# Kernel optimization log

Hardware: AMD Instinct MI355X
Metric: run time of the kernel (lower is better)

Reference implementation:

```python
import jax, jax.numpy as jnp
import numpy as np

N_NODES = 50000
N_EDGES = 600000
N_PAIRS = 200000
D_IN, D_HID = 128, 256


def _sage_conv(x, src, dst, W_l, b_l, W_r, num_nodes):
    # PyG SAGEConv('mean'): out = mean_agg(x_j) @ W_l + b_l + x @ W_r
    msgs = x[src]                                              # [E, d] gather
    agg = jax.ops.segment_sum(msgs, dst, num_segments=num_nodes)
    deg = jax.ops.segment_sum(jnp.ones((src.shape[0],), x.dtype), dst,
                              num_segments=num_nodes)
    agg = agg / jnp.maximum(deg, 1.0)[:, None]                 # mean, safe for deg=0
    return agg @ W_l + b_l + x @ W_r


def setup_inputs() -> dict:
    key = jax.random.key(0)
    ks = jax.random.split(key, 8)
    s = lambda d: 1.0 / np.sqrt(d)
    return {
        "features": jax.random.normal(ks[0], (N_NODES, D_IN), jnp.float32),
        "edge_index": jax.random.randint(ks[1], (2, N_EDGES), 0, N_NODES, jnp.int64),
        "mask": jax.random.randint(ks[2], (N_PAIRS, 2), 0, N_NODES, jnp.int64),
        "W1l": jax.random.normal(ks[3], (D_IN, D_HID), jnp.float32) * s(D_IN),
        "b1l": jnp.zeros((D_HID,), jnp.float32),
        "W1r": jax.random.normal(ks[4], (D_IN, D_HID), jnp.float32) * s(D_IN),
        "W2l": jax.random.normal(ks[5], (D_HID, D_IN), jnp.float32) * s(D_HID),
        "b2l": jnp.zeros((D_IN,), jnp.float32),
        "W2r": jax.random.normal(ks[6], (D_HID, D_IN), jnp.float32) * s(D_HID),
        "Wlin": jax.random.normal(ks[7], (2 * D_IN, 1), jnp.float32) * s(2 * D_IN),
        "blin": jnp.zeros((1,), jnp.float32),
    }


def reference(features, edge_index, mask, W1l, b1l, W1r, W2l, b2l, W2r, Wlin, blin):
    n = features.shape[0]
    src, dst = edge_index[0], edge_index[1]
    h = _sage_conv(features, src, dst, W1l, b1l, W1r, n)       # [N, 256]
    h = jax.nn.relu(h)                                         # dropout p=0 -> identity
    h = _sage_conv(h, src, dst, W2l, b2l, W2r, n)              # [N, 128]
    m = mask.T                                                 # [2, P]
    p1 = jax.lax.stop_gradient(h[m[0]])                        # detach in original
    p2 = jax.lax.stop_gradient(h[m[1]])
    pair = jnp.concatenate((p1, p2), axis=1)                   # [P, 256]
    return jax.nn.sigmoid(pair @ Wlin + blin)                  # [P, 1]
```

## Files before the change

kernel.cpp:

```cpp
#include <hip/hip_runtime.h>
#include <math.h>

#define NN 50000
#define NE 600000
#define NP 200000
#define NB_SCAN 49

typedef unsigned int uint;
typedef unsigned short ushort;
typedef __attribute__((ext_vector_type(8))) short bf16x8;
typedef __attribute__((ext_vector_type(4))) float f32x4;

__device__ __forceinline__ ushort f2bf(float f) {
    uint u = __float_as_uint(f);
    uint r = (u + 0x7FFFu + ((u >> 16) & 1u)) >> 16;
    return (ushort)r;
}
__device__ __forceinline__ float bf2f(uint lo16) {
    return __uint_as_float(lo16 << 16);
}

__device__ __forceinline__ int wave_iscan(int v, int lane) {
#pragma unroll
    for (int off = 1; off < 64; off <<= 1) {
        int t = __shfl_up(v, off, 64);
        if (lane >= off) v += t;
    }
    return v;
}

template <int K, int N>
__device__ __forceinline__ void prepB_one(int idx, const float* __restrict__ Wt,
                                          const float* __restrict__ Wb,
                                          ushort* __restrict__ Bp) {
    int lane = idx & 63;
    int nt = (idx >> 6) % (N / 16);
    int ct = idx / (64 * (N / 16));
    int n = nt * 16 + (lane & 15);
    int kb = ct * 32 + (lane >> 4) * 8;
#pragma unroll
    for (int j = 0; j < 8; j++) {
        int k = kb + j;
        float w = (k < K / 2) ? Wt[(size_t)k * N + n] : Wb[(size_t)(k - K / 2) * N + n];
        Bp[(size_t)idx * 8 + j] = f2bf(w);
    }
}

#define T_PREP (NN * 64)
#define T_DEG  (T_PREP + NE)
#define T_B1   (T_DEG + 8192)
#define T_PQ   (T_B1 + 1024)
#define T_CAB  (T_PQ + 2)
__global__ void k_pre(const float* __restrict__ x, uint* __restrict__ A1u,
                      const int* __restrict__ dst, int* __restrict__ deg,
                      const float* __restrict__ W1l, const float* __restrict__ W1r,
                      ushort* __restrict__ Bp1,
                      const float* __restrict__ W2l, const float* __restrict__ W2r,
                      const float* __restrict__ Wlin, const float* __restrict__ b2l,
                      float* __restrict__ pq, float* __restrict__ cab) {
    int t = blockIdx.x * 256 + threadIdx.x;
    if (t < T_PREP) {
        int n = t >> 6, c2 = t & 63;
        float2 v = *(const float2*)(x + (size_t)n * 128 + c2 * 2);
        A1u[(size_t)n * 128 + 64 + c2] = (uint)f2bf(v.x) | ((uint)f2bf(v.y) << 16);
    } else if (t < T_DEG) {
        atomicAdd(deg + dst[t - T_PREP], 1);
    } else if (t < T_B1) {
        prepB_one<256, 256>(t - T_DEG, W1l, W1r, Bp1);
    } else if (t < T_PQ) {
        int idx = t - T_B1;
        int vec = idx >> 8;
        int k = idx & 255;
        const float* W = (vec < 2) ? W2l : W2r;
        const float* wl = Wlin + (vec & 1) * 128;
        float s = 0.f;
#pragma unroll 4
        for (int j = 0; j < 128; j++) s += W[(size_t)k * 128 + j] * wl[j];
        pq[idx] = s;
    } else if (t < T_CAB) {
        int i = t - T_PQ;
        float s = 0.f;
        for (int j = 0; j < 128; j++) s += b2l[j] * Wlin[i * 128 + j];
        cab[i] = s;
    }
}

__global__ __launch_bounds__(1024) void k_scan1(const int* __restrict__ deg,
                                                int* __restrict__ excl,
                                                int* __restrict__ bsum) {
    int tid = threadIdx.x;
    int i = blockIdx.x * 1024 + tid;
    int lane = tid & 63, wid = tid >> 6;
    int v = (i < NN) ? deg[i] : 0;
    int incl = wave_iscan(v, lane);
    __shared__ int wt[16];
    if (lane == 63) wt[wid] = incl;
    __syncthreads();
    if (tid < 16) {
        int w = wt[tid];
#pragma unroll
        for (int off = 1; off < 16; off <<= 1) {
            int t = __shfl_up(w, off, 64);
            if (tid >= off) w += t;
        }
        wt[tid] = w;
    }
    __syncthreads();
    int base = (wid > 0) ? wt[wid - 1] : 0;
    if (i < NN) excl[i] = incl - v + base;
    if (tid == 0) bsum[blockIdx.x] = wt[15];
}

__global__ void k_scan2(int* __restrict__ bsum) {
    int lane = threadIdx.x;
    int v = (lane < NB_SCAN) ? bsum[lane] : 0;
    int incl = wave_iscan(v, lane);
    if (lane < NB_SCAN) bsum[lane] = incl - v;
}

__global__ __launch_bounds__(1024) void k_scan3(const int* __restrict__ excl,
                                                const int* __restrict__ bsum,
                                                int* __restrict__ rowptr,
                                                int* __restrict__ cursor) {
    int i = blockIdx.x * 1024 + threadIdx.x;
    if (i < NN) {
        int v = excl[i] + bsum[blockIdx.x];
        rowptr[i] = v;
        cursor[i] = v;
    }
    if (i == 0) rowptr[NN] = NE;
}

__global__ void k_fill(const int* __restrict__ src, const int* __restrict__ dst,
                       int* __restrict__ cursor, int* __restrict__ ssrc) {
    int e = blockIdx.x * 256 + threadIdx.x;
    if (e >= NE) return;
    int d = dst[e];
    int pos = atomicAdd(cursor + d, 1);
    ssrc[pos] = src[e];
}

__global__ void k_agg1(uint* __restrict__ A1u, const int* __restrict__ rowptr,
                       const int* __restrict__ ssrc) {
    int t = blockIdx.x * 256 + threadIdx.x;
    int n = t >> 6;
    if (n >= NN) return;
    int lane = t & 63;
    int r0 = rowptr[n], r1 = rowptr[n + 1];
    float ax0 = 0.f, ay0 = 0.f, ax1 = 0.f, ay1 = 0.f;
    float ax2 = 0.f, ay2 = 0.f, ax3 = 0.f, ay3 = 0.f;
    int e = r0;
    for (; e + 4 <= r1; e += 4) {
        int s0 = ssrc[e], s1 = ssrc[e + 1], s2 = ssrc[e + 2], s3 = ssrc[e + 3];
        uint v0 = A1u[(size_t)s0 * 128 + 64 + lane];
        uint v1 = A1u[(size_t)s1 * 128 + 64 + lane];
        uint v2 = A1u[(size_t)s2 * 128 + 64 + lane];
        uint v3 = A1u[(size_t)s3 * 128 + 64 + lane];
        ax0 += bf2f(v0 & 0xffffu); ay0 += bf2f(v0 >> 16);
        ax1 += bf2f(v1 & 0xffffu); ay1 += bf2f(v1 >> 16);
        ax2 += bf2f(v2 & 0xffffu); ay2 += bf2f(v2 >> 16);
        ax3 += bf2f(v3 & 0xffffu); ay3 += bf2f(v3 >> 16);
    }
    for (; e < r1; e++) {
        int s = ssrc[e];
        uint v = A1u[(size_t)s * 128 + 64 + lane];
        ax0 += bf2f(v & 0xffffu); ay0 += bf2f(v >> 16);
    }
    float ax = (ax0 + ax1) + (ax2 + ax3);
    float ay = (ay0 + ay1) + (ay2 + ay3);
    float sc = 1.0f / fmaxf((float)(r1 - r0), 1.0f);
    A1u[(size_t)n * 128 + lane] = (uint)f2bf(ax * sc) | ((uint)f2bf(ay * sc) << 16);
}

__global__ __launch_bounds__(256) void k_gemm1(const ushort* __restrict__ A,
                                               const ushort* __restrict__ Bp,
                                               const float* __restrict__ bias,
                                               const float* __restrict__ pq,
                                               float2* __restrict__ g2,
                                               float2* __restrict__ u2) {
    const int K = 256, NTW = 4;
    int wave = threadIdx.x >> 6;
    int lane = threadIdx.x & 63;
    int quad = lane >> 4;
    int l15 = lane & 15;
    int mbase = blockIdx.x * 32;
    int r0 = mbase + l15;       if (r0 >= NN) r0 = NN - 1;
    int r1 = mbase + 16 + l15;  if (r1 >= NN) r1 = NN - 1;
    f32x4 acc0[NTW], acc1[NTW];
#pragma unroll
    for (int i = 0; i < NTW; i++) {
        acc0[i] = (f32x4){0.f, 0.f, 0.f, 0.f};
        acc1[i] = (f32x4){0.f, 0.f, 0.f, 0.f};
    }
    const bf16x8* bp = (const bf16x8*)Bp;
#pragma unroll
    for (int ct = 0; ct < K / 32; ct++) {
        bf16x8 a0 = *(const bf16x8*)(A + (size_t)r0 * K + ct * 32 + quad * 8);
        bf16x8 a1 = *(const bf16x8*)(A + (size_t)r1 * K + ct * 32 + quad * 8);
#pragma unroll
        for (int ntl = 0; ntl < NTW; ntl++) {
            int nt = wave * NTW + ntl;
            bf16x8 b = bp[(ct * 16 + nt) * 64 + lane];
            acc0[ntl] = __builtin_amdgcn_mfma_f32_16x16x32_bf16(a0, b, acc0[ntl], 0, 0, 0);
            acc1[ntl] = __builtin_amdgcn_mfma_f32_16x16x32_bf16(a1, b, acc1[ntl], 0, 0, 0);
        }
    }
    float pga[2][4] = {{0,0,0,0},{0,0,0,0}}, pgb[2][4] = {{0,0,0,0},{0,0,0,0}};
    float pua[2][4] = {{0,0,0,0},{0,0,0,0}}, pub[2][4] = {{0,0,0,0},{0,0,0,0}};
#pragma unroll
    for (int ntl = 0; ntl < NTW; ntl++) {
        int col = (wave * NTW + ntl) * 16 + l15;
        float bv = bias[col];
        float wpa = pq[col], wpb = pq[256 + col];
        float wqa = pq[512 + col], wqb = pq[768 + col];
#pragma unroll
        for (int reg = 0; reg < 4; reg++) {
            float v0 = acc0[ntl][reg] + bv;  v0 = v0 > 0.f ? v0 : 0.f;
            float v1 = acc1[ntl][reg] + bv;  v1 = v1 > 0.f ? v1 : 0.f;
            pga[0][reg] += v0 * wpa;  pgb[0][reg] += v0 * wpb;
            pua[0][reg] += v0 * wqa;  pub[0][reg] += v0 * wqb;
            pga[1][reg] += v1 * wpa;  pgb[1][reg] += v1 * wpb;
            pua[1][reg] += v1 * wqa;  pub[1][reg] += v1 * wqb;
        }
    }
#pragma unroll
    for (int off = 1; off < 16; off <<= 1) {
#pragma unroll
        for (int rt = 0; rt < 2; rt++) {
#pragma unroll
            for (int reg = 0; reg < 4; reg++) {
                pga[rt][reg] += __shfl_xor(pga[rt][reg], off, 64);
                pgb[rt][reg] += __shfl_xor(pgb[rt][reg], off, 64);
                pua[rt][reg] += __shfl_xor(pua[rt][reg], off, 64);
                pub[rt][reg] += __shfl_xor(pub[rt][reg], off, 64);
            }
        }
    }
    __shared__ float red[4][4][32];
    if (l15 == 0) {
#pragma unroll
        for (int rt = 0; rt < 2; rt++) {
#pragma unroll
            for (int reg = 0; reg < 4; reg++) {
                int row = rt * 16 + quad * 4 + reg;
                red[0][wave][row] = pga[rt][reg];
                red[1][wave][row] = pgb[rt][reg];
                red[2][wave][row] = pua[rt][reg];
                red[3][wave][row] = pub[rt][reg];
            }
        }
    }
    __syncthreads();
    if (threadIdx.x < 32) {
        int row = threadIdx.x;
        int m = mbase + row;
        if (m < NN) {
            float ga = (red[0][0][row] + red[0][1][row]) + (red[0][2][row] + red[0][3][row]);
            float gb = (red[1][0][row] + red[1][1][row]) + (red[1][2][row] + red[1][3][row]);
            float ua = (red[2][0][row] + red[2][1][row]) + (red[2][2][row] + red[2][3][row]);
            float ub = (red[3][0][row] + red[3][1][row]) + (red[3][2][row] + red[3][3][row]);
            g2[m] = make_float2(ga, gb);
            u2[m] = make_float2(ua, ub);
        }
    }
}

__global__ void k_sagg(const float2* __restrict__ g2, const float2* __restrict__ u2,
                       const int* __restrict__ rowptr, const int* __restrict__ ssrc,
                       const float* __restrict__ cab,
                       float* __restrict__ sa, float* __restrict__ sb) {
    int n = blockIdx.x * 256 + threadIdx.x;
    if (n >= NN) return;
    int r0 = rowptr[n], r1 = rowptr[n + 1];
    float a0 = 0.f, b0 = 0.f, a1 = 0.f, b1 = 0.f;
    float a2 = 0.f, b2 = 0.f, a3 = 0.f, b3 = 0.f;
    int e = r0;
    for (; e + 4 <= r1; e += 4) {
        float2 v0 = g2[ssrc[e]];
        float2 v1 = g2[ssrc[e + 1]];
        float2 v2 = g2[ssrc[e + 2]];
        float2 v3 = g2[ssrc[e + 3]];
        a0 += v0.x; b0 += v0.y;
        a1 += v1.x; b1 += v1.y;
        a2 += v2.x; b2 += v2.y;
        a3 += v3.x; b3 += v3.y;
    }
    for (; e < r1; e++) {
        float2 v = g2[ssrc[e]];
        a0 += v.x; b0 += v.y;
    }
    float sc = 1.0f / fmaxf((float)(r1 - r0), 1.0f);
    float2 u = u2[n];
    sa[n] = ((a0 + a1) + (a2 + a3)) * sc + u.x + cab[0];
    sb[n] = ((b0 + b1) + (b2 + b3)) * sc + u.y + cab[1];
}

__global__ void k_pairs(const float* __restrict__ sa, const float* __restrict__ sb,
                        const int* __restrict__ mask, const float* __restrict__ blin,
                        float* __restrict__ out) {
    int p = blockIdx.x * 256 + threadIdx.x;
    if (p >= NP) return;
    int2 m = ((const int2*)mask)[p];
    float v = sa[m.x] + sb[m.y] + blin[0];
    out[p] = 1.0f / (1.0f + __expf(-v));
}

extern "C" void kernel_launch(void* const* d_in, const int* in_sizes, int n_in,
                              void* d_out, int out_size, void* d_ws, size_t ws_size,
                              hipStream_t stream) {
    const float* x    = (const float*)d_in[0];
    const int*   ei   = (const int*)  d_in[1];
    const int*   mask = (const int*)  d_in[2];
    const float* W1l  = (const float*)d_in[3];
    const float* b1l  = (const float*)d_in[4];
    const float* W1r  = (const float*)d_in[5];
    const float* W2l  = (const float*)d_in[6];
    const float* b2l  = (const float*)d_in[7];
    const float* W2r  = (const float*)d_in[8];
    const float* Wlin = (const float*)d_in[9];
    const float* blin = (const float*)d_in[10];
    float* out = (float*)d_out;

    const int* src = ei;
    const int* dst = ei + NE;

    char* ws = (char*)d_ws;
    int*    deg    = (int*)(ws);
    int*    rowptr = (int*)(ws + (size_t)1 * (1 << 20));
    int*    cursor = (int*)(ws + (size_t)2 * (1 << 20));
    int*    ssrc   = (int*)(ws + (size_t)3 * (1 << 20));
    int*    excl   = (int*)(ws + (size_t)6 * (1 << 20));
    int*    bsum   = (int*)(ws + (size_t)7 * (1 << 20));
    ushort* Bp1    = (ushort*)(ws + (size_t)8 * (1 << 20));
    float*  pq     = (float*)(ws + (size_t)9 * (1 << 20));
    float*  cab    = (float*)(ws + (size_t)9 * (1 << 20) + 65536);
    float*  sa     = (float*)(ws + (size_t)10 * (1 << 20));
    float*  sb     = (float*)(ws + (size_t)11 * (1 << 20));
    float2* g2     = (float2*)(ws + (size_t)12 * (1 << 20));
    float2* u2     = (float2*)(ws + (size_t)13 * (1 << 20));
    uint*   A1u    = (uint*)(ws + (size_t)14 * (1 << 20));

    hipMemsetAsync(deg, 0, (size_t)NN * 4, stream);

    k_pre  <<<(T_CAB + 255) / 256, 256, 0, stream>>>(x, A1u, dst, deg,
                                                     W1l, W1r, Bp1,
                                                     W2l, W2r, Wlin, b2l, pq, cab);
    k_scan1<<<NB_SCAN, 1024, 0, stream>>>(deg, excl, bsum);
    k_scan2<<<1, 64, 0, stream>>>(bsum);
    k_scan3<<<NB_SCAN, 1024, 0, stream>>>(excl, bsum, rowptr, cursor);
    k_fill <<<(NE + 255) / 256, 256, 0, stream>>>(src, dst, cursor, ssrc);

    k_agg1 <<<NN / 4, 256, 0, stream>>>(A1u, rowptr, ssrc);
    k_gemm1<<<(NN + 31) / 32, 256, 0, stream>>>((const ushort*)A1u, Bp1, b1l,
                                                pq, g2, u2);
    k_sagg <<<(NN + 255) / 256, 256, 0, stream>>>(g2, u2, rowptr, ssrc, cab, sa, sb);
    k_pairs<<<(NP + 255) / 256, 256, 0, stream>>>(sa, sb, mask, blin, out);
}
```

Before: 226.5 us.

## Merge scan2 into scan3, vectorize feature conversion, unroll aggregation by eight

Three independent tweaks. The single-wave block-sum scan is folded into the final scan kernel, with each block redundantly scanning the 49 block sums, which removes one kernel launch. The bf16 conversion of input features now has each thread handle four floats with a float4 load and a uint2 store. The layer-1 gather loop is unrolled to eight edges so more loads are in flight, at the cost of extra registers.

Measured after the change: 224.8 us. Within noise of the previous version (-0.7%).

```diff
diff --git a/kernel.cpp b/kernel.cpp
--- a/kernel.cpp
+++ b/kernel.cpp
@@ -46,7 +46,7 @@
     }
 }
 
-#define T_PREP (NN * 64)
+#define T_PREP (NN * 32)
 #define T_DEG  (T_PREP + NE)
 #define T_B1   (T_DEG + 8192)
 #define T_PQ   (T_B1 + 1024)
@@ -60,9 +60,12 @@
                       float* __restrict__ pq, float* __restrict__ cab) {
     int t = blockIdx.x * 256 + threadIdx.x;
     if (t < T_PREP) {
-        int n = t >> 6, c2 = t & 63;
-        float2 v = *(const float2*)(x + (size_t)n * 128 + c2 * 2);
-        A1u[(size_t)n * 128 + 64 + c2] = (uint)f2bf(v.x) | ((uint)f2bf(v.y) << 16);
+        int n = t >> 5, c4 = t & 31;
+        float4 v = *(const float4*)(x + (size_t)n * 128 + c4 * 4);
+        uint2 o;
+        o.x = (uint)f2bf(v.x) | ((uint)f2bf(v.y) << 16);
+        o.y = (uint)f2bf(v.z) | ((uint)f2bf(v.w) << 16);
+        *(uint2*)(A1u + (size_t)n * 128 + 64 + c4 * 2) = o;
     } else if (t < T_DEG) {
         atomicAdd(deg + dst[t - T_PREP], 1);
     } else if (t < T_B1) {
@@ -111,20 +114,21 @@
     if (tid == 0) bsum[blockIdx.x] = wt[15];
 }
 
-__global__ void k_scan2(int* __restrict__ bsum) {
-    int lane = threadIdx.x;
-    int v = (lane < NB_SCAN) ? bsum[lane] : 0;
-    int incl = wave_iscan(v, lane);
-    if (lane < NB_SCAN) bsum[lane] = incl - v;
-}
-
-__global__ __launch_bounds__(1024) void k_scan3(const int* __restrict__ excl,
-                                                const int* __restrict__ bsum,
-                                                int* __restrict__ rowptr,
-                                                int* __restrict__ cursor) {
-    int i = blockIdx.x * 1024 + threadIdx.x;
+__global__ __launch_bounds__(1024) void k_scan23(const int* __restrict__ excl,
+                                                 const int* __restrict__ bsum,
+                                                 int* __restrict__ rowptr,
+                                                 int* __restrict__ cursor) {
+    __shared__ int boff;
+    int tid = threadIdx.x;
+    if (tid < 64) {
+        int v = (tid < NB_SCAN) ? bsum[tid] : 0;
+        int incl = wave_iscan(v, tid);
+        if (tid == (int)blockIdx.x) boff = incl - v;
+    }
+    __syncthreads();
+    int i = blockIdx.x * 1024 + tid;
     if (i < NN) {
-        int v = excl[i] + bsum[blockIdx.x];
+        int v = excl[i] + boff;
         rowptr[i] = v;
         cursor[i] = v;
     }
@@ -150,20 +154,26 @@
     float ax0 = 0.f, ay0 = 0.f, ax1 = 0.f, ay1 = 0.f;
     float ax2 = 0.f, ay2 = 0.f, ax3 = 0.f, ay3 = 0.f;
     int e = r0;
-    for (; e + 4 <= r1; e += 4) {
-        int s0 = ssrc[e], s1 = ssrc[e + 1], s2 = ssrc[e + 2], s3 = ssrc[e + 3];
-        uint v0 = A1u[(size_t)s0 * 128 + 64 + lane];
-        uint v1 = A1u[(size_t)s1 * 128 + 64 + lane];
-        uint v2 = A1u[(size_t)s2 * 128 + 64 + lane];
-        uint v3 = A1u[(size_t)s3 * 128 + 64 + lane];
+    for (; e + 8 <= r1; e += 8) {
+        uint v0 = A1u[(size_t)ssrc[e]     * 128 + 64 + lane];
+        uint v1 = A1u[(size_t)ssrc[e + 1] * 128 + 64 + lane];
+        uint v2 = A1u[(size_t)ssrc[e + 2] * 128 + 64 + lane];
+        uint v3 = A1u[(size_t)ssrc[e + 3] * 128 + 64 + lane];
+        uint v4 = A1u[(size_t)ssrc[e + 4] * 128 + 64 + lane];
+        uint v5 = A1u[(size_t)ssrc[e + 5] * 128 + 64 + lane];
+        uint v6 = A1u[(size_t)ssrc[e + 6] * 128 + 64 + lane];
+        uint v7 = A1u[(size_t)ssrc[e + 7] * 128 + 64 + lane];
         ax0 += bf2f(v0 & 0xffffu); ay0 += bf2f(v0 >> 16);
         ax1 += bf2f(v1 & 0xffffu); ay1 += bf2f(v1 >> 16);
         ax2 += bf2f(v2 & 0xffffu); ay2 += bf2f(v2 >> 16);
         ax3 += bf2f(v3 & 0xffffu); ay3 += bf2f(v3 >> 16);
+        ax0 += bf2f(v4 & 0xffffu); ay0 += bf2f(v4 >> 16);
+        ax1 += bf2f(v5 & 0xffffu); ay1 += bf2f(v5 >> 16);
+        ax2 += bf2f(v6 & 0xffffu); ay2 += bf2f(v6 >> 16);
+        ax3 += bf2f(v7 & 0xffffu); ay3 += bf2f(v7 >> 16);
     }
     for (; e < r1; e++) {
-        int s = ssrc[e];
-        uint v = A1u[(size_t)s * 128 + 64 + lane];
+        uint v = A1u[(size_t)ssrc[e] * 128 + 64 + lane];
         ax0 += bf2f(v & 0xffffu); ay0 += bf2f(v >> 16);
     }
     float ax = (ax0 + ax1) + (ax2 + ax3);
@@ -342,17 +352,16 @@
 
     hipMemsetAsync(deg, 0, (size_t)NN * 4, stream);
 
-    k_pre  <<<(T_CAB + 255) / 256, 256, 0, stream>>>(x, A1u, dst, deg,
-                                                     W1l, W1r, Bp1,
-                                                     W2l, W2r, Wlin, b2l, pq, cab);
-    k_scan1<<<NB_SCAN, 1024, 0, stream>>>(deg, excl, bsum);
-    k_scan2<<<1, 64, 0, stream>>>(bsum);
-    k_scan3<<<NB_SCAN, 1024, 0, stream>>>(excl, bsum, rowptr, cursor);
-    k_fill <<<(NE + 255) / 256, 256, 0, stream>>>(src, dst, cursor, ssrc);
-
-    k_agg1 <<<NN / 4, 256, 0, stream>>>(A1u, rowptr, ssrc);
-    k_gemm1<<<(NN + 31) / 32, 256, 0, stream>>>((const ushort*)A1u, Bp1, b1l,
-                                                pq, g2, u2);
-    k_sagg <<<(NN + 255) / 256, 256, 0, stream>>>(g2, u2, rowptr, ssrc, cab, sa, sb);
-    k_pairs<<<(NP + 255) / 256, 256, 0, stream>>>(sa, sb, mask, blin, out);
-}
+    k_pre   <<<(T_CAB + 255) / 256, 256, 0, stream>>>(x, A1u, dst, deg,
+                                                      W1l, W1r, Bp1,
+                                                      W2l, W2r, Wlin, b2l, pq, cab);
+    k_scan1 <<<NB_SCAN, 1024, 0, stream>>>(deg, excl, bsum);
+    k_scan23<<<NB_SCAN, 1024, 0, stream>>>(excl, bsum, rowptr, cursor);
+    k_fill  <<<(NE + 255) / 256, 256, 0, stream>>>(src, dst, cursor, ssrc);
+
+    k_agg1  <<<NN / 4, 256, 0, stream>>>(A1u, rowptr, ssrc);
+    k_gemm1 <<<(NN + 31) / 32, 256, 0, stream>>>((const ushort*)A1u, Bp1, b1l,
+                                                 pq, g2, u2);
+    k_sagg  <<<(NN + 255) / 256, 256, 0, stream>>>(g2, u2, rowptr, ssrc, cab, sa, sb);
+    k_pairs <<<(NP + 255) / 256, 256, 0, stream>>>(sa, sb, mask, blin, out);
+}
```
